# Kernel optimization log

Measured on AMD Instinct MI355X. Metric: run time of the kernel, lower is better.

## Reference

```python
import jax, jax.numpy as jnp
import numpy as np

H_SIZE = 2048
N_HEADS = 16
N_KV = 8
HEAD_DIM = 128
INTER = 8192
WINDOW = 1024
ROPE_BASE = 10000.0
EPS = 1e-6
import math
LAYER_SCALAR_INIT = math.sqrt(1.0 / 8)


def rms_norm(x, w, eps=EPS):
    var = jnp.mean(x * x, axis=-1, keepdims=True)
    return x * jax.lax.rsqrt(var + eps) * w


def rope(x, pos):
    # x: [B,S,H,D], pos: [S]
    half = HEAD_DIM // 2
    inv_freq = 1.0 / (ROPE_BASE ** (jnp.arange(0, HEAD_DIM, 2, dtype=jnp.float32) / HEAD_DIM))
    freqs = pos[:, None].astype(jnp.float32) * inv_freq[None, :]  # [S, D/2]
    cos = jnp.concatenate([jnp.cos(freqs), jnp.cos(freqs)], axis=-1)[None, :, None, :]
    sin = jnp.concatenate([jnp.sin(freqs), jnp.sin(freqs)], axis=-1)[None, :, None, :]
    x1, x2 = x[..., :half], x[..., half:]
    rot = jnp.concatenate([-x2, x1], axis=-1)
    return x * cos + rot * sin


def setup_inputs() -> dict:
    key = jax.random.key(0)
    ks = jax.random.split(key, 12)
    B, S = 2, 2048
    std = 0.02
    return {
        "x": jax.random.normal(ks[0], (B, S, H_SIZE), dtype=jnp.float32),
        "wq": jax.random.normal(ks[1], (N_HEADS * HEAD_DIM, H_SIZE), dtype=jnp.float32) * std,
        "wk": jax.random.normal(ks[2], (N_KV * HEAD_DIM, H_SIZE), dtype=jnp.float32) * std,
        "wv": jax.random.normal(ks[3], (N_KV * HEAD_DIM, H_SIZE), dtype=jnp.float32) * std,
        "wo": jax.random.normal(ks[4], (H_SIZE, N_HEADS * HEAD_DIM), dtype=jnp.float32) * std,
        "w_in_norm": jnp.ones((H_SIZE,), jnp.float32),
        "w_post_attn_norm": jnp.ones((H_SIZE,), jnp.float32),
        "w_pre_ffn_norm": jnp.ones((H_SIZE,), jnp.float32),
        "w_post_ffn_norm": jnp.ones((H_SIZE,), jnp.float32),
        "w_gate": jax.random.normal(ks[5], (INTER, H_SIZE), dtype=jnp.float32) * std,
        "w_up": jax.random.normal(ks[6], (INTER, H_SIZE), dtype=jnp.float32) * std,
        "w_down": jax.random.normal(ks[7], (H_SIZE, INTER), dtype=jnp.float32) * std,
        "layer_scalar": jnp.full((1,), LAYER_SCALAR_INIT, dtype=jnp.float32),
    }


def _block(x, wq, wk, wv, wo, w_in_norm, w_post_attn_norm, w_pre_ffn_norm,
           w_post_ffn_norm, w_gate, w_up, w_down, layer_scalar):
    B, S, _ = x.shape
    h = rms_norm(x, w_in_norm)

    # --- sliding-window GQA attention with RoPE ---
    q = (h @ wq.T).reshape(B, S, N_HEADS, HEAD_DIM)
    k = (h @ wk.T).reshape(B, S, N_KV, HEAD_DIM)
    v = (h @ wv.T).reshape(B, S, N_KV, HEAD_DIM)
    pos = jnp.arange(S)
    q = rope(q, pos)
    k = rope(k, pos)
    group = N_HEADS // N_KV
    k = jnp.repeat(k, group, axis=2)  # [B,S,H,D]
    v = jnp.repeat(v, group, axis=2)
    scale = 1.0 / jnp.sqrt(jnp.float32(HEAD_DIM))
    scores = jnp.einsum('bihd,bjhd->bhij', q, k) * scale  # [B,H,S,S]
    i = pos[:, None]
    j = pos[None, :]
    mask = (j <= i) & (i - j < WINDOW)  # causal sliding window
    scores = jnp.where(mask[None, None], scores, jnp.finfo(scores.dtype).min)
    probs = jax.nn.softmax(scores, axis=-1)
    attn = jnp.einsum('bhij,bjhd->bihd', probs, v).reshape(B, S, N_HEADS * HEAD_DIM)
    attn_out = attn @ wo.T

    h = x + rms_norm(attn_out, w_post_attn_norm)

    # --- GeGLU FFN (exact gelu, matching F.gelu default) ---
    ffn_in = rms_norm(h, w_pre_ffn_norm)
    gate = jax.nn.gelu(ffn_in @ w_gate.T, approximate=False)
    up = ffn_in @ w_up.T
    ffn_out = (gate * up) @ w_down.T
    h = h + rms_norm(ffn_out, w_post_ffn_norm)

    return h * layer_scalar


def reference(x, wq, wk, wv, wo, w_in_norm, w_post_attn_norm, w_pre_ffn_norm,
              w_post_ffn_norm, w_gate, w_up, w_down, layer_scalar):
    return _block(x, wq, wk, wv, wo, w_in_norm, w_post_attn_norm, w_pre_ffn_norm,
                  w_post_ffn_norm, w_gate, w_up, w_down, layer_scalar)
```

## Files before the change

### kernel.cpp

```cpp
#include <hip/hip_runtime.h>


typedef unsigned short u16;
typedef __attribute__((ext_vector_type(4))) float f32x4;
typedef __attribute__((ext_vector_type(8))) short bf16x8;

#define HSZ   2048
#define NH    16
#define NKV   8
#define HD    128
#define INTER 8192
#define SEQ   2048
#define BATCH 2
#define MTOK  (BATCH*SEQ)
#define WIN   1024

__device__ __forceinline__ u16 f2bf(float f) {
    union { float f; unsigned int u; } c; c.f = f;
    unsigned int u = c.u;
    u += 0x7fffu + ((u >> 16) & 1u);
    return (u16)(u >> 16);
}
__device__ __forceinline__ float bf2f(u16 v) {
    union { unsigned int u; float f; } c; c.u = ((unsigned int)v) << 16;
    return c.f;
}
__device__ __forceinline__ float sq4(float4 v) {
    return v.x*v.x + v.y*v.y + v.z*v.z + v.w*v.w;
}
__device__ __forceinline__ void async_ld16(const void* g, void* l) {
    __builtin_amdgcn_global_load_lds(
        (const __attribute__((address_space(1))) void*)g,
        (__attribute__((address_space(3))) void*)l, 16, 0, 0);
}
__device__ __forceinline__ unsigned lds_addr(const void* p) {
    return (unsigned)(unsigned long long)(const __attribute__((address_space(3))) void*)p;
}
template <int OFF>
__device__ __forceinline__ bf16x8 ds_read128(unsigned a) {
    bf16x8 r;
    asm volatile("ds_read_b128 %0, %1 offset:%2" : "=v"(r) : "v"(a), "n"(OFF));
    return r;
}
__device__ __forceinline__ float fast_erf(float x) {
    float ax = fabsf(x);
    float t = 1.0f / (1.0f + 0.3275911f * ax);
    float y = t * (0.254829592f + t * (-0.284496736f + t * (1.421413741f +
              t * (-1.453152027f + t * 1.061405429f))));
    float e = 1.0f - y * __expf(-x * x);
    return copysignf(e, x);
}

__global__ __launch_bounds__(256) void cvt_f32_bf16_k(const float* __restrict__ src,
                                                      u16* __restrict__ dst, int n4) {
    int i = blockIdx.x * 256 + threadIdx.x;
    if (i >= n4) return;
    float4 v = ((const float4*)src)[i];
    ushort4 o;
    o.x = f2bf(v.x); o.y = f2bf(v.y); o.z = f2bf(v.z); o.w = f2bf(v.w);
    ((ushort4*)dst)[i] = o;
}

__global__ __launch_bounds__(256) void cvt_gu_k(const float* __restrict__ wg,
                                                const float* __restrict__ wu,
                                                u16* __restrict__ dst) {
    long i4 = ((long)blockIdx.x * 256 + threadIdx.x) * 4;
    int r = (int)(i4 >> 11);
    int c = (int)(i4 & 2047);
    const float* srow = ((r & 1) ? wu : wg) + (long)(r >> 1) * HSZ + c;
    float4 v = *(const float4*)srow;
    ushort4 o;
    o.x = f2bf(v.x); o.y = f2bf(v.y); o.z = f2bf(v.z); o.w = f2bf(v.w);
    *(ushort4*)(dst + i4) = o;
}

__global__ __launch_bounds__(256) void rmsnorm_bf16_k(const float* __restrict__ x,
                                                      const float* __restrict__ w,
                                                      u16* __restrict__ out) {
    const int row = blockIdx.x, t = threadIdx.x;
    __shared__ float sb[4];
    const float4* xr = (const float4*)(x + (long)row * HSZ);
    float4 v0 = xr[t], v1 = xr[t + 256];
    float ss = sq4(v0) + sq4(v1);
#pragma unroll
    for (int o = 32; o; o >>= 1) ss += __shfl_xor(ss, o);
    if ((t & 63) == 0) sb[t >> 6] = ss;
    __syncthreads();
    ss = sb[0] + sb[1] + sb[2] + sb[3];
    const float rs = rsqrtf(ss * (1.f / HSZ) + 1e-6f);
    const float4* wr = (const float4*)w;
    float4 w0 = wr[t], w1 = wr[t + 256];
    ushort4 o0, o1;
    o0.x = f2bf(v0.x * rs * w0.x); o0.y = f2bf(v0.y * rs * w0.y);
    o0.z = f2bf(v0.z * rs * w0.z); o0.w = f2bf(v0.w * rs * w0.w);
    o1.x = f2bf(v1.x * rs * w1.x); o1.y = f2bf(v1.y * rs * w1.y);
    o1.z = f2bf(v1.z * rs * w1.z); o1.w = f2bf(v1.w * rs * w1.w);
    ushort4* orow = (ushort4*)(out + (long)row * HSZ);
    orow[t] = o0; orow[t + 256] = o1;
}


#define VM_WAIT(n) asm volatile("s_waitcnt vmcnt(" #n ")" ::: "memory")
#define LGKM0      asm volatile("s_waitcnt lgkmcnt(0)" ::: "memory")
#define SBAR       __builtin_amdgcn_s_barrier()
#define SCHED0     __builtin_amdgcn_sched_barrier(0)

#define STAGE_A(pb_, kt_) { \
    const u16* s_ = Ag + (long)(kt_) * 32; \
    u16* d_ = (u16*)As + (pb_) * ATILE + (wave << 9); \
    async_ld16(s_, d_); \
    async_ld16(s_ + (long)128 * K, d_ + 4096); }

#define STAGE_B(pb_, kt_) { \
    const u16* s_ = Bg + (long)(kt_) * 32; \
    u16* d_ = (u16*)Bs + (pb_) * BTILE + (wave << 9); \
    async_ld16(s_, d_); \
    if constexpr (NF == 4) { async_ld16(s_ + (long)128 * K, d_ + 4096); } }

#define KTILE(t_, DOSTAGE_, VMW_) { \
    const unsigned abuf_ = aAb + (unsigned)(((t_) & 3) * (ATILE * 2)); \
    const unsigned bbuf_ = aBb + (unsigned)(((t_) & 3) * (BTILE * 2)); \
    const int pf_ = (t_) + 3; \
    const int pb_ = pf_ & 3; \
    bf16x8 af[4]; \
     \
    af[0] = ds_read128<0>(abuf_);    af[1] = ds_read128<1024>(abuf_); \
    af[2] = ds_read128<2048>(abuf_); af[3] = ds_read128<3072>(abuf_); \
    bfr[0] = ds_read128<0>(bbuf_);   bfr[1] = ds_read128<1024>(bbuf_); \
    if constexpr (NF == 4) { \
        bfr[2] = ds_read128<2048>(bbuf_); bfr[3] = ds_read128<3072>(bbuf_); } \
    if (DOSTAGE_) { STAGE_A(pb_, pf_); } \
    SCHED0; SBAR; LGKM0; SCHED0; \
    __builtin_amdgcn_s_setprio(1); \
    _Pragma("unroll") \
    for (int mi = 0; mi < 4; ++mi) \
        _Pragma("unroll") \
        for (int ni = 0; ni < NF; ++ni) \
            acc[mi][ni] = __builtin_amdgcn_mfma_f32_16x16x32_bf16( \
                af[mi], bfr[ni], acc[mi][ni], 0, 0, 0); \
    __builtin_amdgcn_s_setprio(0); \
    SCHED0; SBAR; SCHED0; \
     \
    af[0] = ds_read128<4096>(abuf_); af[1] = ds_read128<5120>(abuf_); \
    af[2] = ds_read128<6144>(abuf_); af[3] = ds_read128<7168>(abuf_); \
    if (DOSTAGE_) { STAGE_B(pb_, pf_); } \
    SCHED0; VMW_; \
    SCHED0; SBAR; LGKM0; SCHED0; \
    __builtin_amdgcn_s_setprio(1); \
    _Pragma("unroll") \
    for (int mi = 0; mi < 4; ++mi) \
        _Pragma("unroll") \
        for (int ni = 0; ni < NF; ++ni) \
            acc[4 + mi][ni] = __builtin_amdgcn_mfma_f32_16x16x32_bf16( \
                af[mi], bfr[ni], acc[4 + mi][ni], 0, 0, 0); \
    __builtin_amdgcn_s_setprio(0); \
    SCHED0; SBAR; SCHED0; \
}

template <int NF, int EPI>
__global__ __launch_bounds__(512, 2) void gemm_pipe(const u16* __restrict__ A,
                                                    const u16* __restrict__ Bw,
                                                    u16* __restrict__ outp,
                                                    int N, int K) {
    constexpr int BN    = NF * 64;
    constexpr int ATILE = 256 * 32;
    constexpr int BTILE = BN * 32;
    __shared__ alignas(16) u16 As[4 * ATILE];
    __shared__ alignas(16) u16 Bs[4 * BTILE];

    const int tid  = threadIdx.x;
    const int wave = tid >> 6;
    const int lane = tid & 63;
    const int wm   = wave >> 2;
    const int wn   = wave & 3;

    const int nwg  = gridDim.x * gridDim.y;
    const int orig = blockIdx.y * gridDim.x + blockIdx.x;
    const int swz  = (orig & 7) * (nwg >> 3) + (orig >> 3);
    const int m0   = (swz % gridDim.x) << 8;
    const int n0   = (swz / gridDim.x) * BN;

    const int lrow = lane & 15;
    const int px   = (((lane >> 4) ^ ((lrow >> 1) & 3)) << 3);
    const int aoff = ((wm << 7) + lrow) * 32 + px;
    const int boff = (wn * (NF * 16) + lrow) * 32 + px;
    const unsigned aAb = lds_addr(As) + (unsigned)(aoff * 2);
    const unsigned aBb = lds_addr(Bs) + (unsigned)(boff * 2);

    const int srow = tid >> 2;
    const int scol = (((tid & 3) ^ ((tid >> 3) & 3)) << 3);
    const u16* Ag = A  + (long)(m0 + srow) * K + scol;
    const u16* Bg = Bw + (long)(n0 + srow) * K + scol;

    f32x4 acc[8][NF] = {};
    bf16x8 bfr[NF];

    const int NT = K >> 5;

    STAGE_A(0, 0); STAGE_B(0, 0);
    STAGE_A(1, 1); STAGE_B(1, 1);
    STAGE_A(2, 2); STAGE_B(2, 2);
    SCHED0;
    if constexpr (NF == 4) { VM_WAIT(8); } else { VM_WAIT(6); }
    SBAR; SCHED0;

    for (int t = 0; t < NT - 3; ++t) {
        if constexpr (NF == 4) { KTILE(t, 1, VM_WAIT(8)); }
        else                   { KTILE(t, 1, VM_WAIT(6)); }
    }
    if constexpr (NF == 4) { KTILE((NT - 3), 0, VM_WAIT(4)); }
    else                   { KTILE((NT - 3), 0, VM_WAIT(3)); }
    KTILE((NT - 2), 0, VM_WAIT(0));
    KTILE((NT - 1), 0, ((void)0));

    const int drow = (lane >> 4) << 2;
    if constexpr (EPI == 1) {
#pragma unroll
        for (int mi8 = 0; mi8 < 8; ++mi8) {
            const int rb = m0 + (wm << 7) + ((mi8 >> 2) << 6) + ((mi8 & 3) << 4) + drow;
#pragma unroll
            for (int ni = 0; ni < NF; ++ni) {
                const int col = n0 + wn * (NF * 16) + ni * 16 + lrow;
#pragma unroll
                for (int r = 0; r < 4; ++r)
                    outp[(long)(rb + r) * N + col] = f2bf(acc[mi8][ni][r]);
            }
        }
    } else {
        const int No = N >> 1;
#pragma unroll
        for (int mi8 = 0; mi8 < 8; ++mi8) {
            const int rb = m0 + (wm << 7) + ((mi8 >> 2) << 6) + ((mi8 & 3) << 4) + drow;
#pragma unroll
            for (int ni = 0; ni < NF; ni += 2) {
                const int colown = n0 + wn * 64 + (ni + (lane & 1)) * 16 + lrow;
#pragma unroll
                for (int r = 0; r < 4; ++r) {
                    float a = acc[mi8][ni][r];
                    float b = acc[mi8][ni + 1][r];
                    float a1 = __shfl_xor(a, 1);
                    float b1 = __shfl_xor(b, 1);
                    float g = (lane & 1) ? b1 : a;
                    float u = (lane & 1) ? b  : a1;
                    float act = 0.5f * g * (1.f + fast_erf(g * 0.70710678f)) * u;
                    outp[(long)(rb + r) * No + (colown >> 1)] = f2bf(act);
                }
            }
        }
    }
}

__global__ __launch_bounds__(128) void rope_repack_k(const u16* __restrict__ qkv,
                                                     u16* __restrict__ Qh,
                                                     u16* __restrict__ Kh) {
    const int m = blockIdx.x;
    const int slot = blockIdx.y;
    const int d = threadIdx.x;
    const int b = m >> 11, s = m & 2047;
    const int colbase = (slot < 16) ? (slot << 7) : (2048 + ((slot - 16) << 7));
    const float xv = bf2f(qkv[(long)m * 4096 + colbase + d]);
    const float xp = bf2f(qkv[(long)m * 4096 + colbase + (d ^ 64)]);
    const int i = d & 63;
    const float inv = exp2f(-(float)i * 0.20762050593045864f);
    const float fr = (float)s * inv;
    const float cs = cosf(fr), sn = sinf(fr);
    const float ov = (d < 64) ? (xv * cs - xp * sn) : (xv * cs + xp * sn);
    if (slot < 16) {
        Qh[(((long)(b * NH + slot)) * SEQ + s) * HD + d] = f2bf(ov);
    } else {
        Kh[(((long)(b * NKV + (slot - 16))) * SEQ + s) * HD + d] = f2bf(ov);
    }
}

__global__ __launch_bounds__(256) void v_transpose_k(const u16* __restrict__ qkv,
                                                     u16* __restrict__ Vt) {
    __shared__ alignas(16) u16 tile[64][130];
    const int st = blockIdx.x, g = blockIdx.y, b = blockIdx.z;
    const int s0 = st * 64;
    const int tid = threadIdx.x;
#pragma unroll
    for (int i = 0; i < 32; ++i) {
        int idx = i * 256 + tid;
        int sl = idx >> 7, d = idx & 127;
        tile[sl][d] = qkv[(long)(b * SEQ + s0 + sl) * 4096 + 3072 + g * 128 + d];
    }
    __syncthreads();
#pragma unroll
    for (int i = 0; i < 32; ++i) {
        int idx = i * 256 + tid;
        int d = idx >> 6, sl = idx & 63;
        Vt[((long)(b * NKV + g) * HD + d) * SEQ + s0 + sl] = tile[sl][d];
    }
}

__global__ __launch_bounds__(256) void flash_attn_k(const u16* __restrict__ Qh,
                                                    const u16* __restrict__ Kh,
                                                    const u16* __restrict__ Vt,
                                                    u16* __restrict__ attn) {
    __shared__ alignas(16) u16 Qs[64 * 128];
    __shared__ alignas(16) u16 Ks[64 * 128];
    __shared__ alignas(16) u16 Vts[128 * 64];
    __shared__ alignas(16) u16 Ps[4][16 * 64];
    const int tid = threadIdx.x;
    const int wave = tid >> 6, lane = tid & 63;
    const int qt = blockIdx.x, h = blockIdx.y, b = blockIdx.z;
    const int g = h >> 1;
    const int q0 = qt * 64;
    const u16* Qg = Qh + (((long)(b * NH + h) * SEQ) + q0) * HD;
    const u16* Kg = Kh + ((long)(b * NKV + g) * SEQ) * HD;
    const u16* Vg = Vt + ((long)(b * NKV + g) * HD) * SEQ;

    {
        const int4* src = (const int4*)Qg;
        int4* dst = (int4*)Qs;
#pragma unroll
        for (int i = 0; i < 4; ++i) dst[tid + i * 256] = src[tid + i * 256];
    }
    __syncthreads();
    const int lrow = lane & 15;
    const int kq = (lane >> 4) << 3;
    bf16x8 aq[4];
#pragma unroll
    for (int ks = 0; ks < 4; ++ks)
        aq[ks] = *(const bf16x8*)(Qs + (wave * 16 + lrow) * 128 + ks * 32 + kq);

    f32x4 o[8] = {};
    float mrow[4], lsum[4];
#pragma unroll
    for (int r = 0; r < 4; ++r) { mrow[r] = -1e30f; lsum[r] = 0.f; }

    const int jlo = (q0 - (WIN - 1)) > 0 ? (q0 - (WIN - 1)) : 0;
    const int t0 = jlo >> 6, t1 = q0 >> 6;
    for (int jt = t0; jt <= t1; ++jt) {
        const int j0 = jt * 64;
        __syncthreads();
        {
            const int4* src = (const int4*)(Kg + (long)j0 * HD);
            int4* dst = (int4*)Ks;
#pragma unroll
            for (int i = 0; i < 4; ++i) dst[tid + i * 256] = src[tid + i * 256];
        }
        {
            const int row = tid >> 1, half = tid & 1;
            const int4* src = (const int4*)(Vg + (long)row * SEQ + j0 + half * 32);
            int4* dst = (int4*)(Vts + row * 64 + half * 32);
#pragma unroll
            for (int i = 0; i < 4; ++i) dst[i] = src[i];
        }
        __syncthreads();

        f32x4 sc[4];
#pragma unroll
        for (int nt = 0; nt < 4; ++nt) {
            f32x4 s = {};
#pragma unroll
            for (int ks = 0; ks < 4; ++ks) {
                bf16x8 bk = *(const bf16x8*)(Ks + (nt * 16 + lrow) * 128 + ks * 32 + kq);
                s = __builtin_amdgcn_mfma_f32_16x16x32_bf16(aq[ks], bk, s, 0, 0, 0);
            }
            sc[nt] = s;
        }

        const int qbase = q0 + wave * 16 + ((lane >> 4) << 2);
        float pv[4][4];
#pragma unroll
        for (int r = 0; r < 4; ++r) {
            const int qi = qbase + r;
            float mx = -1e30f;
#pragma unroll
            for (int nt = 0; nt < 4; ++nt) {
                const int ki = j0 + nt * 16 + lrow;
                float s = sc[nt][r] * 0.08838834764831845f;
                bool valid = (ki <= qi) && (qi - ki < WIN);
                s = valid ? s : -1e30f;
                sc[nt][r] = s;
                mx = fmaxf(mx, s);
            }
            mx = fmaxf(mx, __shfl_xor(mx, 1));
            mx = fmaxf(mx, __shfl_xor(mx, 2));
            mx = fmaxf(mx, __shfl_xor(mx, 4));
            mx = fmaxf(mx, __shfl_xor(mx, 8));
            const float mn = fmaxf(mrow[r], mx);
            const float alpha = __expf(mrow[r] - mn);
            float rsum = 0.f;
#pragma unroll
            for (int nt = 0; nt < 4; ++nt) {
                float s = sc[nt][r];
                float p = (s > -1e29f) ? __expf(s - mn) : 0.f;
                pv[nt][r] = p;
                rsum += p;
            }
            rsum += __shfl_xor(rsum, 1);
            rsum += __shfl_xor(rsum, 2);
            rsum += __shfl_xor(rsum, 4);
            rsum += __shfl_xor(rsum, 8);
            lsum[r] = lsum[r] * alpha + rsum;
            mrow[r] = mn;
#pragma unroll
            for (int dt = 0; dt < 8; ++dt) o[dt][r] *= alpha;
        }

        u16* myP = (u16*)Ps[wave];
#pragma unroll
        for (int r = 0; r < 4; ++r) {
            const int prow = ((lane >> 4) << 2) + r;
#pragma unroll
            for (int nt = 0; nt < 4; ++nt)
                myP[prow * 64 + nt * 16 + lrow] = f2bf(pv[nt][r]);
        }
        __syncthreads();

#pragma unroll
        for (int kst = 0; kst < 2; ++kst) {
            bf16x8 ap = *(const bf16x8*)(myP + lrow * 64 + kst * 32 + kq);
#pragma unroll
            for (int dt = 0; dt < 8; ++dt) {
                bf16x8 bv = *(const bf16x8*)(Vts + (dt * 16 + lrow) * 64 + kst * 32 + kq);
                o[dt] = __builtin_amdgcn_mfma_f32_16x16x32_bf16(ap, bv, o[dt], 0, 0, 0);
            }
        }
    }

#pragma unroll
    for (int r = 0; r < 4; ++r) {
        const int qi = q0 + wave * 16 + ((lane >> 4) << 2) + r;
        const float inv = 1.f / lsum[r];
        const long mrowg = (long)b * SEQ + qi;
#pragma unroll
        for (int dt = 0; dt < 8; ++dt)
            attn[mrowg * (NH * HD) + h * 128 + dt * 16 + lrow] = f2bf(o[dt][r] * inv);
    }
}

__global__ __launch_bounds__(256) void addnorm2_k(const float* __restrict__ x,
                                                  const u16* __restrict__ ao,
                                                  const float* __restrict__ wpost,
                                                  const float* __restrict__ wpre,
                                                  u16* __restrict__ h2,
                                                  u16* __restrict__ ffin) {
    const int row = blockIdx.x, t = threadIdx.x;
    __shared__ float sb[4];
    const long base = (long)row * HSZ;
    ushort4 a4_0 = ((const ushort4*)(ao + base))[t];
    ushort4 a4_1 = ((const ushort4*)(ao + base))[t + 256];
    float4 a0, a1;
    a0.x = bf2f(a4_0.x); a0.y = bf2f(a4_0.y); a0.z = bf2f(a4_0.z); a0.w = bf2f(a4_0.w);
    a1.x = bf2f(a4_1.x); a1.y = bf2f(a4_1.y); a1.z = bf2f(a4_1.z); a1.w = bf2f(a4_1.w);
    float ss = sq4(a0) + sq4(a1);
#pragma unroll
    for (int o = 32; o; o >>= 1) ss += __shfl_xor(ss, o);
    if ((t & 63) == 0) sb[t >> 6] = ss;
    __syncthreads();
    ss = sb[0] + sb[1] + sb[2] + sb[3];
    const float rs1 = rsqrtf(ss * (1.f / HSZ) + 1e-6f);

    const float4* xr = (const float4*)(x + base);
    float4 x0 = xr[t], x1 = xr[t + 256];
    float4 wp0 = ((const float4*)wpost)[t], wp1 = ((const float4*)wpost)[t + 256];
    float4 h0, h1;
    h0.x = x0.x + a0.x * rs1 * wp0.x; h0.y = x0.y + a0.y * rs1 * wp0.y;
    h0.z = x0.z + a0.z * rs1 * wp0.z; h0.w = x0.w + a0.w * rs1 * wp0.w;
    h1.x = x1.x + a1.x * rs1 * wp1.x; h1.y = x1.y + a1.y * rs1 * wp1.y;
    h1.z = x1.z + a1.z * rs1 * wp1.z; h1.w = x1.w + a1.w * rs1 * wp1.w;
    ushort4 hb0, hb1;
    hb0.x = f2bf(h0.x); hb0.y = f2bf(h0.y); hb0.z = f2bf(h0.z); hb0.w = f2bf(h0.w);
    hb1.x = f2bf(h1.x); hb1.y = f2bf(h1.y); hb1.z = f2bf(h1.z); hb1.w = f2bf(h1.w);
    ((ushort4*)(h2 + base))[t] = hb0;
    ((ushort4*)(h2 + base))[t + 256] = hb1;

    float ss2 = sq4(h0) + sq4(h1);
#pragma unroll
    for (int o = 32; o; o >>= 1) ss2 += __shfl_xor(ss2, o);
    __syncthreads();
    if ((t & 63) == 0) sb[t >> 6] = ss2;
    __syncthreads();
    ss2 = sb[0] + sb[1] + sb[2] + sb[3];
    const float rs2 = rsqrtf(ss2 * (1.f / HSZ) + 1e-6f);
    float4 wq0 = ((const float4*)wpre)[t], wq1 = ((const float4*)wpre)[t + 256];
    ushort4 o0, o1;
    o0.x = f2bf(h0.x * rs2 * wq0.x); o0.y = f2bf(h0.y * rs2 * wq0.y);
    o0.z = f2bf(h0.z * rs2 * wq0.z); o0.w = f2bf(h0.w * rs2 * wq0.w);
    o1.x = f2bf(h1.x * rs2 * wq1.x); o1.y = f2bf(h1.y * rs2 * wq1.y);
    o1.z = f2bf(h1.z * rs2 * wq1.z); o1.w = f2bf(h1.w * rs2 * wq1.w);
    ushort4* fr = (ushort4*)(ffin + base);
    fr[t] = o0; fr[t + 256] = o1;
}

__global__ __launch_bounds__(256) void final_k(const u16* __restrict__ h2,
                                               const u16* __restrict__ fo,
                                               const float* __restrict__ wpost,
                                               const float* __restrict__ lscal,
                                               float* __restrict__ out) {
    const int row = blockIdx.x, t = threadIdx.x;
    __shared__ float sb[4];
    const long base = (long)row * HSZ;
    ushort4 f4_0 = ((const ushort4*)(fo + base))[t];
    ushort4 f4_1 = ((const ushort4*)(fo + base))[t + 256];
    float4 f0, f1;
    f0.x = bf2f(f4_0.x); f0.y = bf2f(f4_0.y); f0.z = bf2f(f4_0.z); f0.w = bf2f(f4_0.w);
    f1.x = bf2f(f4_1.x); f1.y = bf2f(f4_1.y); f1.z = bf2f(f4_1.z); f1.w = bf2f(f4_1.w);
    float ss = sq4(f0) + sq4(f1);
#pragma unroll
    for (int o = 32; o; o >>= 1) ss += __shfl_xor(ss, o);
    if ((t & 63) == 0) sb[t >> 6] = ss;
    __syncthreads();
    ss = sb[0] + sb[1] + sb[2] + sb[3];
    const float rs = rsqrtf(ss * (1.f / HSZ) + 1e-6f);
    const float sc = lscal[0];
    ushort4 h4_0 = ((const ushort4*)(h2 + base))[t];
    ushort4 h4_1 = ((const ushort4*)(h2 + base))[t + 256];
    float4 wp0 = ((const float4*)wpost)[t], wp1 = ((const float4*)wpost)[t + 256];
    float4 r0, r1;
    r0.x = (bf2f(h4_0.x) + f0.x * rs * wp0.x) * sc;
    r0.y = (bf2f(h4_0.y) + f0.y * rs * wp0.y) * sc;
    r0.z = (bf2f(h4_0.z) + f0.z * rs * wp0.z) * sc;
    r0.w = (bf2f(h4_0.w) + f0.w * rs * wp0.w) * sc;
    r1.x = (bf2f(h4_1.x) + f1.x * rs * wp1.x) * sc;
    r1.y = (bf2f(h4_1.y) + f1.y * rs * wp1.y) * sc;
    r1.z = (bf2f(h4_1.z) + f1.z * rs * wp1.z) * sc;
    r1.w = (bf2f(h4_1.w) + f1.w * rs * wp1.w) * sc;
    ((float4*)(out + base))[t] = r0;
    ((float4*)(out + base))[t + 256] = r1;
}

extern "C" void kernel_launch(void* const* d_in, const int* in_sizes, int n_in,
                              void* d_out, int out_size, void* d_ws, size_t ws_size,
                              hipStream_t stream) {
    (void)in_sizes; (void)n_in; (void)out_size;
    const float* x     = (const float*)d_in[0];
    const float* wq    = (const float*)d_in[1];
    const float* wk    = (const float*)d_in[2];
    const float* wv    = (const float*)d_in[3];
    const float* wo    = (const float*)d_in[4];
    const float* w_in  = (const float*)d_in[5];
    const float* w_pa  = (const float*)d_in[6];
    const float* w_pf  = (const float*)d_in[7];
    const float* w_pff = (const float*)d_in[8];
    const float* wgate = (const float*)d_in[9];
    const float* wup   = (const float*)d_in[10];
    const float* wdown = (const float*)d_in[11];
    const float* lscal = (const float*)d_in[12];
    float* out = (float*)d_out;

    const size_t NEED = 276824064ull;
    if (ws_size < NEED) return;
    char* ws = (char*)d_ws;
    u16* Wqkv  = (u16*)(ws);
    u16* Wo    = (u16*)(ws + 16777216);
    u16* Wgu   = (u16*)(ws + 25165824);
    u16* Wdown = (u16*)(ws + 92274688);
    u16* act   = (u16*)(ws + 125829120);
    u16* R1    = (u16*)(ws + 192937984);
    u16* R2    = (u16*)(ws + 226492416);
    u16* R3    = (u16*)(ws + 260046848);
    u16* qkvb = R1;
    u16* aout = R1;
    u16* ffin = R1 + 8388608;
    u16* fout = R1 + 8388608;
    u16* Qh = R2;
    u16* Kh = R2 + 8388608;
    u16* Vt = R2 + 12582912;
    u16* h2 = R2;
    u16* hnorm = R3;
    u16* attn  = R3;

    cvt_f32_bf16_k<<<4096, 256, 0, stream>>>(wq, Wqkv, 2048 * 2048 / 4);
    cvt_f32_bf16_k<<<2048, 256, 0, stream>>>(wk, Wqkv + 2048 * 2048, 1024 * 2048 / 4);
    cvt_f32_bf16_k<<<2048, 256, 0, stream>>>(wv, Wqkv + 3072 * 2048, 1024 * 2048 / 4);
    cvt_f32_bf16_k<<<4096, 256, 0, stream>>>(wo, Wo, 2048 * 2048 / 4);
    cvt_gu_k<<<32768, 256, 0, stream>>>(wgate, wup, Wgu);
    cvt_f32_bf16_k<<<16384, 256, 0, stream>>>(wdown, Wdown, HSZ * INTER / 4);

    rmsnorm_bf16_k<<<MTOK, 256, 0, stream>>>(x, w_in, hnorm);
    gemm_pipe<4, 1><<<dim3(16, 16), 512, 0, stream>>>(hnorm, Wqkv, qkvb, 4096, HSZ);
    rope_repack_k<<<dim3(MTOK, 24), 128, 0, stream>>>(qkvb, Qh, Kh);
    v_transpose_k<<<dim3(SEQ / 64, NKV, BATCH), 256, 0, stream>>>(qkvb, Vt);
    flash_attn_k<<<dim3(SEQ / 64, NH, BATCH), 256, 0, stream>>>(Qh, Kh, Vt, attn);
    gemm_pipe<2, 1><<<dim3(16, 16), 512, 0, stream>>>(attn, Wo, aout, HSZ, HSZ);
    addnorm2_k<<<MTOK, 256, 0, stream>>>(x, aout, w_pa, w_pf, h2, ffin);
    gemm_pipe<4, 2><<<dim3(16, 64), 512, 0, stream>>>(ffin, Wgu, act, 2 * INTER, HSZ);
    gemm_pipe<2, 1><<<dim3(16, 16), 512, 0, stream>>>(act, Wdown, fout, HSZ, INTER);
    final_k<<<MTOK, 256, 0, stream>>>(h2, fout, w_pff, lscal, out);
}
```

Baseline: 1.046 ms.

## Prefetch next K-tile LDS fragments into double-buffered registers, drop barriers

Restructures the GEMM main loop so the A-even and B fragments for the next K-tile are read from LDS during the current tile's MFMAs, using ping-pong register sets (aE/aO, bA/bB) and partial lgkmcnt waits. It also issues both A and B global stages together and removes two of the three barriers per tile. The aim is to hide LDS read latency and barrier stalls behind matrix instructions. In exchange it raises register pressure and relies on the 4-deep LDS ring being large enough that fewer barriers still avoid read/write hazards, with the loop unrolled by two and fixed tail tiles.

```diff
diff --git a/kernel.cpp b/kernel.cpp
--- a/kernel.cpp
+++ b/kernel.cpp
@@ -101,58 +101,56 @@
 
 
 #define VM_WAIT(n) asm volatile("s_waitcnt vmcnt(" #n ")" ::: "memory")
-#define LGKM0      asm volatile("s_waitcnt lgkmcnt(0)" ::: "memory")
+#define LGKM_(n)   asm volatile("s_waitcnt lgkmcnt(" #n ")" ::: "memory")
+#define LGKM(n)    LGKM_(n)
 #define SBAR       __builtin_amdgcn_s_barrier()
 #define SCHED0     __builtin_amdgcn_sched_barrier(0)
 
-#define STAGE_A(pb_, kt_) { \
+#define STAGE_A(kt_) { \
     const u16* s_ = Ag + (long)(kt_) * 32; \
-    u16* d_ = (u16*)As + (pb_) * ATILE + (wave << 9); \
+    u16* d_ = (u16*)As + ((kt_) & 3) * ATILE + (wave << 9); \
     async_ld16(s_, d_); \
     async_ld16(s_ + (long)128 * K, d_ + 4096); }
 
-#define STAGE_B(pb_, kt_) { \
+#define STAGE_B(kt_) { \
     const u16* s_ = Bg + (long)(kt_) * 32; \
-    u16* d_ = (u16*)Bs + (pb_) * BTILE + (wave << 9); \
+    u16* d_ = (u16*)Bs + ((kt_) & 3) * BTILE + (wave << 9); \
     async_ld16(s_, d_); \
     if constexpr (NF == 4) { async_ld16(s_ + (long)128 * K, d_ + 4096); } }
 
-#define KTILE(t_, DOSTAGE_, VMW_) { \
+#define KTILE2(t_, bU_, bP_, DOSTAGE_, VMW_, PREF_, LGO_) { \
     const unsigned abuf_ = aAb + (unsigned)(((t_) & 3) * (ATILE * 2)); \
-    const unsigned bbuf_ = aBb + (unsigned)(((t_) & 3) * (BTILE * 2)); \
-    const int pf_ = (t_) + 3; \
-    const int pb_ = pf_ & 3; \
-    bf16x8 af[4]; \
+    const unsigned anxt_ = aAb + (unsigned)((((t_) + 1) & 3) * (ATILE * 2)); \
+    const unsigned bnxt_ = aBb + (unsigned)((((t_) + 1) & 3) * (BTILE * 2)); \
      \
-    af[0] = ds_read128<0>(abuf_);    af[1] = ds_read128<1024>(abuf_); \
-    af[2] = ds_read128<2048>(abuf_); af[3] = ds_read128<3072>(abuf_); \
-    bfr[0] = ds_read128<0>(bbuf_);   bfr[1] = ds_read128<1024>(bbuf_); \
-    if constexpr (NF == 4) { \
-        bfr[2] = ds_read128<2048>(bbuf_); bfr[3] = ds_read128<3072>(bbuf_); } \
-    if (DOSTAGE_) { STAGE_A(pb_, pf_); } \
-    SCHED0; SBAR; LGKM0; SCHED0; \
+    aO[0] = ds_read128<4096>(abuf_); aO[1] = ds_read128<5120>(abuf_); \
+    aO[2] = ds_read128<6144>(abuf_); aO[3] = ds_read128<7168>(abuf_); \
+    if (DOSTAGE_) { STAGE_A((t_) + 3); STAGE_B((t_) + 3); } \
+    LGKM(4); SCHED0; \
     __builtin_amdgcn_s_setprio(1); \
     _Pragma("unroll") \
     for (int mi = 0; mi < 4; ++mi) \
         _Pragma("unroll") \
         for (int ni = 0; ni < NF; ++ni) \
             acc[mi][ni] = __builtin_amdgcn_mfma_f32_16x16x32_bf16( \
-                af[mi], bfr[ni], acc[mi][ni], 0, 0, 0); \
-    __builtin_amdgcn_s_setprio(0); \
-    SCHED0; SBAR; SCHED0; \
-     \
-    af[0] = ds_read128<4096>(abuf_); af[1] = ds_read128<5120>(abuf_); \
-    af[2] = ds_read128<6144>(abuf_); af[3] = ds_read128<7168>(abuf_); \
-    if (DOSTAGE_) { STAGE_B(pb_, pf_); } \
-    SCHED0; VMW_; \
-    SCHED0; SBAR; LGKM0; SCHED0; \
+                aE[mi], bU_[ni], acc[mi][ni], 0, 0, 0); \
+    __builtin_amdgcn_s_setprio(0); SCHED0; \
+    VMW_; SCHED0; \
+    if (PREF_) {  \
+        aE[0] = ds_read128<0>(anxt_);    aE[1] = ds_read128<1024>(anxt_); \
+        aE[2] = ds_read128<2048>(anxt_); aE[3] = ds_read128<3072>(anxt_); \
+        bP_[0] = ds_read128<0>(bnxt_);   bP_[1] = ds_read128<1024>(bnxt_); \
+        if constexpr (NF == 4) { \
+            bP_[2] = ds_read128<2048>(bnxt_); bP_[3] = ds_read128<3072>(bnxt_); } \
+    } \
+    LGKM(LGO_); SCHED0; \
     __builtin_amdgcn_s_setprio(1); \
     _Pragma("unroll") \
     for (int mi = 0; mi < 4; ++mi) \
         _Pragma("unroll") \
         for (int ni = 0; ni < NF; ++ni) \
             acc[4 + mi][ni] = __builtin_amdgcn_mfma_f32_16x16x32_bf16( \
-                af[mi], bfr[ni], acc[4 + mi][ni], 0, 0, 0); \
+                aO[mi], bU_[ni], acc[4 + mi][ni], 0, 0, 0); \
     __builtin_amdgcn_s_setprio(0); \
     SCHED0; SBAR; SCHED0; \
 }
@@ -193,25 +191,44 @@
     const u16* Bg = Bw + (long)(n0 + srow) * K + scol;
 
     f32x4 acc[8][NF] = {};
-    bf16x8 bfr[NF];
+    bf16x8 aE[4], aO[4], bA[NF], bB[NF];
 
     const int NT = K >> 5;
 
-    STAGE_A(0, 0); STAGE_B(0, 0);
-    STAGE_A(1, 1); STAGE_B(1, 1);
-    STAGE_A(2, 2); STAGE_B(2, 2);
+    STAGE_A(0); STAGE_B(0);
+    STAGE_A(1); STAGE_B(1);
+    STAGE_A(2); STAGE_B(2);
     SCHED0;
-    if constexpr (NF == 4) { VM_WAIT(8); } else { VM_WAIT(6); }
+    if constexpr (NF == 4) { VM_WAIT(4); } else { VM_WAIT(3); }
     SBAR; SCHED0;
-
-    for (int t = 0; t < NT - 3; ++t) {
-        if constexpr (NF == 4) { KTILE(t, 1, VM_WAIT(8)); }
-        else                   { KTILE(t, 1, VM_WAIT(6)); }
-    }
-    if constexpr (NF == 4) { KTILE((NT - 3), 0, VM_WAIT(4)); }
-    else                   { KTILE((NT - 3), 0, VM_WAIT(3)); }
-    KTILE((NT - 2), 0, VM_WAIT(0));
-    KTILE((NT - 1), 0, ((void)0));
+    {
+        const unsigned a0 = aAb, b0 = aBb;
+        aE[0] = ds_read128<0>(a0);    aE[1] = ds_read128<1024>(a0);
+        aE[2] = ds_read128<2048>(a0); aE[3] = ds_read128<3072>(a0);
+        bA[0] = ds_read128<0>(b0);    bA[1] = ds_read128<1024>(b0);
+        if constexpr (NF == 4) {
+            bA[2] = ds_read128<2048>(b0); bA[3] = ds_read128<3072>(b0); }
+    }
+
+    if constexpr (NF == 4) {
+        for (int t = 0; t < NT - 4; t += 2) {
+            KTILE2(t,     bA, bB, 1, VM_WAIT(4), 1, 8);
+            KTILE2(t + 1, bB, bA, 1, VM_WAIT(4), 1, 8);
+        }
+        KTILE2((NT - 4), bA, bB, 1, VM_WAIT(4), 1, 8);
+        KTILE2((NT - 3), bB, bA, 0, VM_WAIT(0), 1, 8);
+        KTILE2((NT - 2), bA, bB, 0, ((void)0),  1, 8);
+        KTILE2((NT - 1), bB, bA, 0, ((void)0),  0, 0);
+    } else {
+        for (int t = 0; t < NT - 4; t += 2) {
+            KTILE2(t,     bA, bB, 1, VM_WAIT(3), 1, 6);
+            KTILE2(t + 1, bB, bA, 1, VM_WAIT(3), 1, 6);
+        }
+        KTILE2((NT - 4), bA, bB, 1, VM_WAIT(3), 1, 6);
+        KTILE2((NT - 3), bB, bA, 0, VM_WAIT(0), 1, 6);
+        KTILE2((NT - 2), bA, bB, 0, ((void)0),  1, 6);
+        KTILE2((NT - 1), bB, bA, 0, ((void)0),  0, 0);
+    }
 
     const int drow = (lane >> 4) << 2;
     if constexpr (EPI == 1) {
```

Result: no change. 1.056 ms (+1.0%).
